# Kernel tuning notes

Hardware: AMD Instinct MI355X
Metric: run time of the kernel (lower is better)

Reference implementation:

```python
import jax, jax.numpy as jnp
import numpy as np

B, N, C_IN, C_H, C_OUT, R, X_DIM = 32, 256, 64, 128, 128, 5, 1024
NEG = -9e15

def _leaky(x, s=0.2):
    return jnp.where(x >= 0, x, s * x)

def gat_layer(atoms, mask, W, b, a):
    # atoms: (B,n,c_in), mask: (B,n,n,R) bool, W: (c_in, R*c), b: (R*c,), a: (R, 2c)
    bs, n, _ = atoms.shape
    c = a.shape[1] // 2
    h = (atoms @ W + b).reshape(bs, n, R, c)            # (B,n,R,c)
    src = jnp.einsum('bnrc,rc->bnr', h, a[:, :c])       # a . h_i part
    dst = jnp.einsum('bnrc,rc->bnr', h, a[:, c:])       # a . h_j part
    logits = _leaky(src[:, :, None, :] + dst[:, None, :, :])  # (B,i,j,R)
    masked = jnp.where(mask, logits, NEG)
    probs = jax.nn.softmax(masked.reshape(bs, n, n * R), axis=2).reshape(bs, n, n, R)
    return jnp.einsum('bijr,bjrc->bic', probs, h)       # (B,n,c)

def setup_inputs() -> dict:
    key = jax.random.key(0)
    ks = jax.random.split(key, 16)
    def p(k, shape, fan):
        return jax.random.normal(k, shape, jnp.float32) * (1.414 / np.sqrt(fan))
    inp = {
        'x': jax.random.normal(ks[0], (B, X_DIM), jnp.float32),
        'y_atoms': jax.random.normal(ks[1], (B, N, C_IN), jnp.float32),
        'y_bonds': jax.random.randint(ks[2], (B, N, N, R), 0, 2, jnp.int32),
        'W1': p(ks[3], (C_IN, R * C_H), C_IN), 'b1': jnp.zeros((R * C_H,), jnp.float32),
        'a1': p(ks[4], (R, 2 * C_H), 2 * C_H),
        'W2': p(ks[5], (C_H, R * C_H), C_H), 'b2': jnp.zeros((R * C_H,), jnp.float32),
        'a2': p(ks[6], (R, 2 * C_H), 2 * C_H),
        'W3': p(ks[7], (C_H, R * C_OUT), C_H), 'b3': jnp.zeros((R * C_OUT,), jnp.float32),
        'a3': p(ks[8], (R, 2 * C_OUT), 2 * C_OUT),
        'We1': p(ks[9], (2 * C_OUT + X_DIM, 256), 2 * C_OUT + X_DIM), 'be1': jnp.zeros((256,), jnp.float32),
        'We2': p(ks[10], (256, 32), 256), 'be2': jnp.zeros((32,), jnp.float32),
        'We3': p(ks[11], (32, 1), 32), 'be3': jnp.zeros((1,), jnp.float32),
    }
    return inp

def reference(x, y_atoms, y_bonds, W1, b1, a1, W2, b2, a2, W3, b3, a3,
              We1, be1, We2, be2, We3, be3):
    mask = (y_bonds == 1)
    h = gat_layer(y_atoms, mask, W1, b1, a1)
    h = _leaky(h)                                   # dropout is identity at eval
    h = gat_layer(h, mask, W2, b2, a2)
    h = _leaky(h)
    h = gat_layer(h, mask, W3, b3, a3)
    y_feats = jnp.concatenate([jnp.mean(h, axis=1), jnp.max(h, axis=1)], axis=1)
    z = jnp.concatenate([x, y_feats], axis=1)
    z = _leaky(z @ We1 + be1)
    z = _leaky(z @ We2 + be2)
    return z @ We3 + be3
```

## Files before the change

kernel.cpp:

```cpp
#include <hip/hip_runtime.h>
#include <cstddef>

typedef __attribute__((ext_vector_type(8))) short bf16x8;
typedef __attribute__((ext_vector_type(4))) float f32x4;

__device__ __forceinline__ float lrelu(float x) { return x >= 0.f ? x : 0.2f * x; }
__device__ __forceinline__ unsigned short f2bf(float x) {
    unsigned u = __float_as_uint(x);
    u += 0x7FFFu + ((u >> 16) & 1u);
    return (unsigned short)(u >> 16);
}

__global__ __launch_bounds__(256) void k_prepw(const float* __restrict__ W1,
                                               unsigned short* __restrict__ WT1) {
    const int nt = blockIdx.x, t = threadIdx.x;
    const int n = nt * 64 + (t & 63);
    for (int kg = t >> 6; kg < 8; kg += 4) {
        bf16x8 v;
#pragma unroll
        for (int e = 0; e < 8; ++e) v[e] = (short)f2bf(W1[(size_t)(kg * 8 + e) * 640 + n]);
        *(bf16x8*)&WT1[(size_t)n * 64 + kg * 8] = v;
    }
}

template <int K, int MODE, int EXTRA>
__global__ __launch_bounds__(256) void k_gemm_h(const float* __restrict__ Af32,
                                                const unsigned short* __restrict__ Ab,
                                                const unsigned short* __restrict__ WTg,
                                                const float* __restrict__ bias,
                                                const float* __restrict__ avec,
                                                float* __restrict__ srcp,
                                                float* __restrict__ dstp,
                                                unsigned short* __restrict__ hTf,
                                                const int* __restrict__ bonds,
                                                unsigned char* __restrict__ maskp,
                                                const float* __restrict__ W2,
                                                const float* __restrict__ W3,
                                                unsigned short* __restrict__ WT2,
                                                unsigned short* __restrict__ WT3) {
    const int t = threadIdx.x;
    const int l = blockIdx.x;
    if (EXTRA && l >= 1280) {
        int e = l - 1280;
        if (e < 2048) {
            int gt = e * 256 + t;
            const int4* p = (const int4*)(bonds + (size_t)gt * 20);
            int4 q0 = p[0], q1 = p[1], q2 = p[2], q3 = p[3], q4 = p[4];
            int v[20] = {q0.x, q0.y, q0.z, q0.w, q1.x, q1.y, q1.z, q1.w,
                         q2.x, q2.y, q2.z, q2.w, q3.x, q3.y, q3.z, q3.w,
                         q4.x, q4.y, q4.z, q4.w};
            unsigned m = 0;
#pragma unroll
            for (int k = 0; k < 4; ++k)
#pragma unroll
                for (int r = 0; r < 5; ++r)
                    m |= (v[k * 5 + r] == 1) ? (1u << (k * 8 + r)) : 0u;
            *(unsigned*)&maskp[(size_t)gt * 4] = m;
        } else {
            int e2 = e - 2048;
            const float* W = (e2 < 10) ? W2 : W3;
            unsigned short* WT = (e2 < 10) ? WT2 : WT3;
            int nt = (e2 < 10) ? e2 : e2 - 10;
            int n = nt * 64 + (t & 63);
            for (int kg = t >> 6; kg < 16; kg += 4) {
                bf16x8 v;
#pragma unroll
                for (int ee = 0; ee < 8; ++ee)
                    v[ee] = (short)f2bf(W[(size_t)(kg * 8 + ee) * 640 + n]);
                *(bf16x8*)&WT[(size_t)n * 128 + kg * 8] = v;
            }
        }
        return;
    }
    const int mt = (l & 7) * 16 + ((l >> 3) & 15);
    const int nt = l >> 7;
    const int n0 = nt * 64, m0 = mt * 64;
    const int w = t >> 6, lane = t & 63;
    const int colg = lane & 15, rquad = lane >> 4;
    const int m = m0 + w * 16 + colg;
    const int koff = rquad * 8;

    f32x4 acc[4] = {};
#pragma unroll
    for (int kk = 0; kk < K; kk += 32) {
        bf16x8 af;
        size_t off = (size_t)m * K + kk + koff;
        if (MODE == 1) {
            af = *(const bf16x8*)&Ab[off];
        } else {
            float4 q0 = *(const float4*)&Af32[off];
            float4 q1 = *(const float4*)&Af32[off + 4];
            af[0] = (short)f2bf(q0.x); af[1] = (short)f2bf(q0.y);
            af[2] = (short)f2bf(q0.z); af[3] = (short)f2bf(q0.w);
            af[4] = (short)f2bf(q1.x); af[5] = (short)f2bf(q1.y);
            af[6] = (short)f2bf(q1.z); af[7] = (short)f2bf(q1.w);
        }
#pragma unroll
        for (int ct = 0; ct < 4; ++ct) {
            bf16x8 bfv = *(const bf16x8*)&WTg[(size_t)(n0 + ct * 16 + colg) * K + kk + koff];
            acc[ct] = __builtin_amdgcn_mfma_f32_16x16x32_bf16(af, bfv, acc[ct], 0, 0, 0);
        }
    }

    const int r = n0 >> 7, chalf = n0 & 127;
    const int b = m0 >> 8, jb = m0 & 255;
    float val[4][4];
    float ssum[4] = {0.f, 0.f, 0.f, 0.f}, dsum[4] = {0.f, 0.f, 0.f, 0.f};
#pragma unroll
    for (int ct = 0; ct < 4; ++ct) {
        int cg = chalf + ct * 16 + colg;
        float bv = bias[n0 + ct * 16 + colg];
        float asr = avec[r * 256 + cg];
        float ads = avec[r * 256 + 128 + cg];
#pragma unroll
        for (int reg = 0; reg < 4; ++reg) {
            float v = acc[ct][reg] + bv;
            val[ct][reg] = v;
            ssum[reg] += v * asr;
            dsum[reg] += v * ads;
        }
    }
#pragma unroll
    for (int mk = 1; mk < 16; mk <<= 1)
#pragma unroll
        for (int reg = 0; reg < 4; ++reg) {
            ssum[reg] += __shfl_xor(ssum[reg], mk);
            dsum[reg] += __shfl_xor(dsum[reg], mk);
        }
    if (colg == 0) {
        int nhalf = (n0 >> 6) & 1;
#pragma unroll
        for (int reg = 0; reg < 4; ++reg) {
            int row = m0 + w * 16 + rquad * 4 + reg;
            srcp[nhalf * 40960 + row * 5 + r] = ssum[reg];
            dstp[nhalf * 40960 + row * 5 + r] = dsum[reg];
        }
    }
    {
        const int joct = (jb >> 3) + w * 2 + (rquad >> 1);
        const size_t tile = (size_t)((b * 5 + r) * 32 + joct) * 1024;
        const int sub = (rquad & 1) * 4;
#pragma unroll
        for (int ct = 0; ct < 4; ++ct) {
            int c = chalf + ct * 16 + colg;
            uint2 pk;
            pk.x = (unsigned)f2bf(val[ct][0]) | ((unsigned)f2bf(val[ct][1]) << 16);
            pk.y = (unsigned)f2bf(val[ct][2]) | ((unsigned)f2bf(val[ct][3]) << 16);
            *(uint2*)&hTf[tile + (size_t)c * 8 + sub] = pk;
        }
    }
}

template <int FINAL>
__global__ __launch_bounds__(512, 4) void k_agg(const unsigned short* __restrict__ hTf,
                                                const float* __restrict__ srcp,
                                                const float* __restrict__ dstp,
                                                const unsigned char* __restrict__ maskp,
                                                unsigned short* __restrict__ Ab,
                                                float* __restrict__ poolS,
                                                float* __restrict__ poolM) {
    __shared__ __align__(16) unsigned short Ps[20480];
    __shared__ __align__(16) float Ds2l[1280];
    __shared__ float Ss[80], Zw[128], Zrow[16];
    const int t = threadIdx.x;
    const int l = blockIdx.x;
    const int b = (l & 7) * 4 + ((l >> 3) & 3);
    const int itile = l >> 5;
    const int ib = b * 256 + itile * 16;
    const int w = t >> 6, lane = t & 63;
    const int colg = lane & 15, rquad = lane >> 4;
    const int c = w * 16 + colg;
    const size_t bbase = (size_t)(b * 5) * 32 * 1024;

    if (t < 80) Ss[t] = srcp[(size_t)ib * 5 + t] + srcp[40960 + (size_t)ib * 5 + t];
    for (int idx = t; idx < 1280; idx += 512) {
        int jl = idx & 255, rr = idx >> 8;
        size_t o = (size_t)(b * 256 + jl) * 5 + rr;
        Ds2l[rr * 256 + jl] = dstp[o] + dstp[40960 + o];
    }
    bf16x8 pre[4];
#pragma unroll
    for (int s = 0; s < 4; ++s)
        pre[s] = *(const bf16x8*)&hTf[bbase + (size_t)(s * 4 + rquad) * 1024 + (size_t)c * 8];
    __syncthreads();

    {
        const int i = t & 15;
        const int kq = (t >> 4) & 3;
        float esum = 0.f;
#pragma unroll
        for (int it = 0; it < 5; ++it) {
            int p = it * 512 + t;
            int s = p >> 6;
            int k0 = s * 32 + kq * 8;
            int rr = k0 >> 8, j0 = k0 & 255;
            uint2 mk8 = *(const uint2*)&maskp[((size_t)(ib + i) << 8) + j0];
            float sv = Ss[i * 5 + rr];
            float4 d0 = *(const float4*)&Ds2l[rr * 256 + j0];
            float4 d1 = *(const float4*)&Ds2l[rr * 256 + j0 + 4];
            float dv[8] = {d0.x, d0.y, d0.z, d0.w, d1.x, d1.y, d1.z, d1.w};
            bf16x8 pv;
#pragma unroll
            for (int e = 0; e < 8; ++e) {
                unsigned mb = ((e < 4 ? (mk8.x >> (8 * e)) : (mk8.y >> (8 * (e - 4)))) >> rr) & 1u;
                float vv = lrelu(sv + dv[e]);
                float ev = mb ? __expf(vv) : 0.f;
                unsigned short q = f2bf(ev);
                pv[e] = (short)q;
                esum += __uint_as_float((unsigned)q << 16);
            }
            *(bf16x8*)&Ps[p * 8] = pv;
        }
        esum += __shfl_xor(esum, 16);
        esum += __shfl_xor(esum, 32);
        if (lane < 16) Zw[w * 16 + (lane & 15)] = esum;
    }
    __syncthreads();
    if (t < 16) {
        float z = 0.f;
#pragma unroll
        for (int ww = 0; ww < 8; ++ww) z += Zw[ww * 16 + t];
        Zrow[t] = 1.f / z;
    }

    f32x4 acc0 = {}, acc1 = {};
#pragma unroll
    for (int s = 0; s < 8; ++s) {
        bf16x8 af = *(const bf16x8*)&Ps[(s * 64 + lane) * 8];
        bf16x8 bfv;
        if (s < 4) bfv = pre[s];
        else bfv = *(const bf16x8*)&hTf[bbase + (size_t)((s & 7) * 4 + rquad) * 1024 + (size_t)c * 8];
        if (s & 1) acc1 = __builtin_amdgcn_mfma_f32_16x16x32_bf16(af, bfv, acc1, 0, 0, 0);
        else       acc0 = __builtin_amdgcn_mfma_f32_16x16x32_bf16(af, bfv, acc0, 0, 0, 0);
    }
#pragma unroll 8
    for (int s = 8; s < 40; ++s) {
        bf16x8 af = *(const bf16x8*)&Ps[(s * 64 + lane) * 8];
        bf16x8 bfv = *(const bf16x8*)&hTf[bbase +
            (size_t)((s >> 3) * 32 + (s & 7) * 4 + rquad) * 1024 + (size_t)c * 8];
        if (s & 1) acc1 = __builtin_amdgcn_mfma_f32_16x16x32_bf16(af, bfv, acc1, 0, 0, 0);
        else       acc0 = __builtin_amdgcn_mfma_f32_16x16x32_bf16(af, bfv, acc0, 0, 0, 0);
    }
    __syncthreads();
    const int irow = ib + rquad * 4;
    if (FINAL) {
        float ps = 0.f, pm = -3.4e38f;
#pragma unroll
        for (int reg = 0; reg < 4; ++reg) {
            float v = (acc0[reg] + acc1[reg]) * Zrow[rquad * 4 + reg];
            ps += v;
            pm = fmaxf(pm, v);
        }
        ps += __shfl_xor(ps, 16);
        ps += __shfl_xor(ps, 32);
        pm = fmaxf(pm, __shfl_xor(pm, 16));
        pm = fmaxf(pm, __shfl_xor(pm, 32));
        if (rquad == 0) {
            poolS[(size_t)(b * 16 + itile) * 128 + c] = ps;
            poolM[(size_t)(b * 16 + itile) * 128 + c] = pm;
        }
    } else {
#pragma unroll
        for (int reg = 0; reg < 4; ++reg) {
            float v = (acc0[reg] + acc1[reg]) * Zrow[rquad * 4 + reg];
            Ab[(size_t)(irow + reg) * 128 + c] = f2bf(lrelu(v));
        }
    }
}

__global__ __launch_bounds__(256) void k_mlp1(const float* __restrict__ x,
                                              const float* __restrict__ poolS,
                                              const float* __restrict__ poolM,
                                              const float* __restrict__ We1,
                                              float* __restrict__ z1p) {
    const int kg = blockIdx.x, b = blockIdx.y;
    const int t = threadIdx.x;
    __shared__ float zs[256];
    if (kg < 4) {
        zs[t] = x[(size_t)b * 1024 + kg * 256 + t];
    } else if (t < 128) {
        float s = 0.f;
#pragma unroll
        for (int it = 0; it < 16; ++it) s += poolS[(size_t)(b * 16 + it) * 128 + t];
        zs[t] = s * (1.f / 256.f);
    } else {
        int f = t - 128;
        float mx = -3.4e38f;
#pragma unroll
        for (int it = 0; it < 16; ++it) mx = fmaxf(mx, poolM[(size_t)(b * 16 + it) * 128 + f]);
        zs[t] = mx;
    }
    __syncthreads();
    float s = 0.f;
#pragma unroll 8
    for (int k = 0; k < 256; ++k) s += zs[k] * We1[(size_t)(kg * 256 + k) * 256 + t];
    z1p[(size_t)(b * 5 + kg) * 256 + t] = s;
}

__global__ __launch_bounds__(256) void k_mlp2(const float* __restrict__ z1p,
                                              const float* __restrict__ be1,
                                              const float* __restrict__ We2,
                                              const float* __restrict__ be2,
                                              const float* __restrict__ We3,
                                              const float* __restrict__ be3,
                                              float* __restrict__ out) {
    const int b = blockIdx.x, t = threadIdx.x;
    __shared__ float z1s[256];
    __shared__ float s2p[8][32];
    __shared__ float z2s[32];
    {
        float s = be1[t];
#pragma unroll
        for (int kg = 0; kg < 5; ++kg) s += z1p[(size_t)(b * 5 + kg) * 256 + t];
        z1s[t] = lrelu(s);
    }
    __syncthreads();
    {
        int o = t & 31, g = t >> 5;
        float p = 0.f;
#pragma unroll
        for (int k = 0; k < 32; ++k) p += z1s[g * 32 + k] * We2[(g * 32 + k) * 32 + o];
        s2p[g][o] = p;
    }
    __syncthreads();
    if (t < 32) {
        float s2 = be2[t];
#pragma unroll
        for (int g = 0; g < 8; ++g) s2 += s2p[g][t];
        z2s[t] = lrelu(s2);
    }
    __syncthreads();
    if (t == 0) {
        float s3 = be3[0];
#pragma unroll
        for (int k = 0; k < 32; ++k) s3 += z2s[k] * We3[k];
        out[b] = s3;
    }
}

constexpr size_t O_MASK  = 0;
constexpr size_t O_SRCP  = 2097152;
constexpr size_t O_DSTP  = O_SRCP + 2ull * 40960 * 4;
constexpr size_t O_AB    = O_DSTP + 2ull * 40960 * 4;
constexpr size_t O_HT    = O_AB + 2097152;
constexpr size_t O_WT1   = O_HT + 5242880ull * 2;
constexpr size_t O_WT2   = O_WT1 + 640ull * 64 * 2;
constexpr size_t O_WT3   = O_WT2 + 640ull * 128 * 2;
constexpr size_t O_POOLS = O_WT3 + 640ull * 128 * 2;
constexpr size_t O_POOLM = O_POOLS + 32ull * 16 * 128 * 4;
constexpr size_t O_Z1P   = O_POOLM + 32ull * 16 * 128 * 4;

extern "C" void kernel_launch(void* const* d_in, const int* in_sizes, int n_in,
                              void* d_out, int out_size, void* d_ws, size_t ws_size,
                              hipStream_t stream) {
    const float* x       = (const float*)d_in[0];
    const float* y_atoms = (const float*)d_in[1];
    const int*   y_bonds = (const int*)d_in[2];
    const float* W1 = (const float*)d_in[3];
    const float* b1 = (const float*)d_in[4];
    const float* a1 = (const float*)d_in[5];
    const float* W2 = (const float*)d_in[6];
    const float* b2 = (const float*)d_in[7];
    const float* a2 = (const float*)d_in[8];
    const float* W3 = (const float*)d_in[9];
    const float* b3 = (const float*)d_in[10];
    const float* a3 = (const float*)d_in[11];
    const float* We1 = (const float*)d_in[12];
    const float* be1 = (const float*)d_in[13];
    const float* We2 = (const float*)d_in[14];
    const float* be2 = (const float*)d_in[15];
    const float* We3 = (const float*)d_in[16];
    const float* be3 = (const float*)d_in[17];
    float* out = (float*)d_out;

    char* ws = (char*)d_ws;
    unsigned char* maskp = (unsigned char*)(ws + O_MASK);
    float* srcp = (float*)(ws + O_SRCP);
    float* dstp = (float*)(ws + O_DSTP);
    unsigned short* Ab = (unsigned short*)(ws + O_AB);
    unsigned short* hTf = (unsigned short*)(ws + O_HT);
    unsigned short* WT1 = (unsigned short*)(ws + O_WT1);
    unsigned short* WT2 = (unsigned short*)(ws + O_WT2);
    unsigned short* WT3 = (unsigned short*)(ws + O_WT3);
    float* poolS = (float*)(ws + O_POOLS);
    float* poolM = (float*)(ws + O_POOLM);
    float* z1p   = (float*)(ws + O_Z1P);

    dim3 blk(256);

    k_prepw<<<10, blk, 0, stream>>>(W1, WT1);

    k_gemm_h<64, 0, 1><<<3348, blk, 0, stream>>>(
        y_atoms, nullptr, WT1, b1, a1, srcp, dstp, hTf,
        y_bonds, maskp, W2, W3, WT2, WT3);
    k_agg<0><<<512, dim3(512), 0, stream>>>(hTf, srcp, dstp, maskp, Ab, nullptr, nullptr);

    k_gemm_h<128, 1, 0><<<1280, blk, 0, stream>>>(
        nullptr, Ab, WT2, b2, a2, srcp, dstp, hTf,
        nullptr, nullptr, nullptr, nullptr, nullptr, nullptr);
    k_agg<0><<<512, dim3(512), 0, stream>>>(hTf, srcp, dstp, maskp, Ab, nullptr, nullptr);

    k_gemm_h<128, 1, 0><<<1280, blk, 0, stream>>>(
        nullptr, Ab, WT3, b3, a3, srcp, dstp, hTf,
        nullptr, nullptr, nullptr, nullptr, nullptr, nullptr);
    k_agg<1><<<512, dim3(512), 0, stream>>>(hTf, srcp, dstp, maskp, nullptr, poolS, poolM);

    k_mlp1<<<dim3(5, 32), blk, 0, stream>>>(x, poolS, poolM, We1, z1p);
    k_mlp2<<<32, blk, 0, stream>>>(z1p, be1, We2, be2, We3, be3, out);
}
```

Baseline: 201.9 us.

## Split aggregation K-loop across 16 waves with LDS reduction of partial accumulators

Doubles the k_agg block to 1024 threads. The two halves of the block each handle half of the 40 MFMA K-steps and combine their partial accumulators through LDS that reuses the probability buffer. The probability-generation loop is redistributed across the larger block, and the register prefetch of the first B fragments is dropped. The aim is more waves in flight per CU to hide the global hTf loads. The cost is an extra LDS round trip and barrier, with half the threads idle in the epilogue.

```diff
diff --git a/kernel.cpp b/kernel.cpp
--- a/kernel.cpp
+++ b/kernel.cpp
@@ -152,16 +152,21 @@
 }
 
 template <int FINAL>
-__global__ __launch_bounds__(512, 4) void k_agg(const unsigned short* __restrict__ hTf,
-                                                const float* __restrict__ srcp,
-                                                const float* __restrict__ dstp,
-                                                const unsigned char* __restrict__ maskp,
-                                                unsigned short* __restrict__ Ab,
-                                                float* __restrict__ poolS,
-                                                float* __restrict__ poolM) {
-    __shared__ __align__(16) unsigned short Ps[20480];
-    __shared__ __align__(16) float Ds2l[1280];
-    __shared__ float Ss[80], Zw[128], Zrow[16];
+__global__ __launch_bounds__(1024, 8) void k_agg(const unsigned short* __restrict__ hTf,
+                                                 const float* __restrict__ srcp,
+                                                 const float* __restrict__ dstp,
+                                                 const unsigned char* __restrict__ maskp,
+                                                 unsigned short* __restrict__ Ab,
+                                                 float* __restrict__ poolS,
+                                                 float* __restrict__ poolM) {
+    __shared__ __align__(16) unsigned char SM[47488];
+    unsigned short* Ps = (unsigned short*)SM;
+    float* accb = (float*)SM;
+    float* Ds2l = (float*)(SM + 40960);
+    float* Ss   = (float*)(SM + 46080);
+    float* Zw   = (float*)(SM + 46400);
+    float* Zrow = (float*)(SM + 47424);
+
     const int t = threadIdx.x;
     const int l = blockIdx.x;
     const int b = (l & 7) * 4 + ((l >> 3) & 3);
@@ -169,19 +174,14 @@
     const int ib = b * 256 + itile * 16;
     const int w = t >> 6, lane = t & 63;
     const int colg = lane & 15, rquad = lane >> 4;
-    const int c = w * 16 + colg;
     const size_t bbase = (size_t)(b * 5) * 32 * 1024;
 
     if (t < 80) Ss[t] = srcp[(size_t)ib * 5 + t] + srcp[40960 + (size_t)ib * 5 + t];
-    for (int idx = t; idx < 1280; idx += 512) {
+    for (int idx = t; idx < 1280; idx += 1024) {
         int jl = idx & 255, rr = idx >> 8;
         size_t o = (size_t)(b * 256 + jl) * 5 + rr;
         Ds2l[rr * 256 + jl] = dstp[o] + dstp[40960 + o];
     }
-    bf16x8 pre[4];
-#pragma unroll
-    for (int s = 0; s < 4; ++s)
-        pre[s] = *(const bf16x8*)&hTf[bbase + (size_t)(s * 4 + rquad) * 1024 + (size_t)c * 8];
     __syncthreads();
 
     {
@@ -189,27 +189,29 @@
         const int kq = (t >> 4) & 3;
         float esum = 0.f;
 #pragma unroll
-        for (int it = 0; it < 5; ++it) {
-            int p = it * 512 + t;
-            int s = p >> 6;
-            int k0 = s * 32 + kq * 8;
-            int rr = k0 >> 8, j0 = k0 & 255;
-            uint2 mk8 = *(const uint2*)&maskp[((size_t)(ib + i) << 8) + j0];
-            float sv = Ss[i * 5 + rr];
-            float4 d0 = *(const float4*)&Ds2l[rr * 256 + j0];
-            float4 d1 = *(const float4*)&Ds2l[rr * 256 + j0 + 4];
-            float dv[8] = {d0.x, d0.y, d0.z, d0.w, d1.x, d1.y, d1.z, d1.w};
-            bf16x8 pv;
-#pragma unroll
-            for (int e = 0; e < 8; ++e) {
-                unsigned mb = ((e < 4 ? (mk8.x >> (8 * e)) : (mk8.y >> (8 * (e - 4)))) >> rr) & 1u;
-                float vv = lrelu(sv + dv[e]);
-                float ev = mb ? __expf(vv) : 0.f;
-                unsigned short q = f2bf(ev);
-                pv[e] = (short)q;
-                esum += __uint_as_float((unsigned)q << 16);
+        for (int it = 0; it < 3; ++it) {
+            int p = it * 1024 + t;
+            if (p < 2560) {
+                int s = p >> 6;
+                int k0 = s * 32 + kq * 8;
+                int rr = k0 >> 8, j0 = k0 & 255;
+                uint2 mk8 = *(const uint2*)&maskp[((size_t)(ib + i) << 8) + j0];
+                float sv = Ss[i * 5 + rr];
+                float4 d0 = *(const float4*)&Ds2l[rr * 256 + j0];
+                float4 d1 = *(const float4*)&Ds2l[rr * 256 + j0 + 4];
+                float dv[8] = {d0.x, d0.y, d0.z, d0.w, d1.x, d1.y, d1.z, d1.w};
+                bf16x8 pv;
+#pragma unroll
+                for (int e = 0; e < 8; ++e) {
+                    unsigned mb = ((e < 4 ? (mk8.x >> (8 * e)) : (mk8.y >> (8 * (e - 4)))) >> rr) & 1u;
+                    float vv = lrelu(sv + dv[e]);
+                    float ev = mb ? __expf(vv) : 0.f;
+                    unsigned short q = f2bf(ev);
+                    pv[e] = (short)q;
+                    esum += __uint_as_float((unsigned)q << 16);
+                }
+                *(bf16x8*)&Ps[p * 8] = pv;
             }
-            *(bf16x8*)&Ps[p * 8] = pv;
         }
         esum += __shfl_xor(esum, 16);
         esum += __shfl_xor(esum, 32);
@@ -219,51 +221,56 @@
     if (t < 16) {
         float z = 0.f;
 #pragma unroll
-        for (int ww = 0; ww < 8; ++ww) z += Zw[ww * 16 + t];
+        for (int ww = 0; ww < 16; ++ww) z += Zw[ww * 16 + t];
         Zrow[t] = 1.f / z;
     }
 
+    const int c = (w & 7) * 16 + colg;
+    const int sbase = (w >> 3) * 20;
     f32x4 acc0 = {}, acc1 = {};
-#pragma unroll
-    for (int s = 0; s < 8; ++s) {
-        bf16x8 af = *(const bf16x8*)&Ps[(s * 64 + lane) * 8];
-        bf16x8 bfv;
-        if (s < 4) bfv = pre[s];
-        else bfv = *(const bf16x8*)&hTf[bbase + (size_t)((s & 7) * 4 + rquad) * 1024 + (size_t)c * 8];
-        if (s & 1) acc1 = __builtin_amdgcn_mfma_f32_16x16x32_bf16(af, bfv, acc1, 0, 0, 0);
-        else       acc0 = __builtin_amdgcn_mfma_f32_16x16x32_bf16(af, bfv, acc0, 0, 0, 0);
-    }
-#pragma unroll 8
-    for (int s = 8; s < 40; ++s) {
+#pragma unroll 4
+    for (int q = 0; q < 20; ++q) {
+        int s = sbase + q;
         bf16x8 af = *(const bf16x8*)&Ps[(s * 64 + lane) * 8];
         bf16x8 bfv = *(const bf16x8*)&hTf[bbase +
             (size_t)((s >> 3) * 32 + (s & 7) * 4 + rquad) * 1024 + (size_t)c * 8];
-        if (s & 1) acc1 = __builtin_amdgcn_mfma_f32_16x16x32_bf16(af, bfv, acc1, 0, 0, 0);
+        if (q & 1) acc1 = __builtin_amdgcn_mfma_f32_16x16x32_bf16(af, bfv, acc1, 0, 0, 0);
         else       acc0 = __builtin_amdgcn_mfma_f32_16x16x32_bf16(af, bfv, acc0, 0, 0, 0);
     }
     __syncthreads();
-    const int irow = ib + rquad * 4;
-    if (FINAL) {
-        float ps = 0.f, pm = -3.4e38f;
-#pragma unroll
-        for (int reg = 0; reg < 4; ++reg) {
-            float v = (acc0[reg] + acc1[reg]) * Zrow[rquad * 4 + reg];
-            ps += v;
-            pm = fmaxf(pm, v);
-        }
-        ps += __shfl_xor(ps, 16);
-        ps += __shfl_xor(ps, 32);
-        pm = fmaxf(pm, __shfl_xor(pm, 16));
-        pm = fmaxf(pm, __shfl_xor(pm, 32));
-        if (rquad == 0) {
-            poolS[(size_t)(b * 16 + itile) * 128 + c] = ps;
-            poolM[(size_t)(b * 16 + itile) * 128 + c] = pm;
-        }
-    } else {
-#pragma unroll
-        for (int reg = 0; reg < 4; ++reg) {
-            float v = (acc0[reg] + acc1[reg]) * Zrow[rquad * 4 + reg];
-            Ab[(size_t)(irow + reg) * 128 + c] = f2bf(lrelu(v));
+    {
+        f32x4 ac;
+#pragma unroll
+        for (int reg = 0; reg < 4; ++reg) ac[reg] = acc0[reg] + acc1[reg];
+        *(f32x4*)&accb[(size_t)(w * 64 + lane) * 4] = ac;
+    }
+    __syncthreads();
+    if (t < 512) {
+        f32x4 pa = *(const f32x4*)&accb[(size_t)(w * 64 + lane) * 4];
+        f32x4 pb = *(const f32x4*)&accb[(size_t)((w + 8) * 64 + lane) * 4];
+        const int irow = ib + rquad * 4;
+        if (FINAL) {
+            float ps = 0.f, pm = -3.4e38f;
+#pragma unroll
+            for (int reg = 0; reg < 4; ++reg) {
+                float v = (pa[reg] + pb[reg]) * Zrow[rquad * 4 + reg];
+                ps += v;
+                pm = fmaxf(pm, v);
+            }
+            ps += __shfl_xor(ps, 16);
+            ps += __shfl_xor(ps, 32);
+            pm = fmaxf(pm, __shfl_xor(pm, 16));
+            pm = fmaxf(pm, __shfl_xor(pm, 32));
+            if (rquad == 0) {
+                poolS[(size_t)(b * 16 + itile) * 128 + c] = ps;
+                poolM[(size_t)(b * 16 + itile) * 128 + c] = pm;
+            }
+        } else {
+#pragma unroll
+            for (int reg = 0; reg < 4; ++reg) {
+                float v = (pa[reg] + pb[reg]) * Zrow[rquad * 4 + reg];
+                Ab[(size_t)(irow + reg) * 128 + c] = f2bf(lrelu(v));
+            }
         }
     }
 }
@@ -393,17 +400,17 @@
     k_gemm_h<64, 0, 1><<<3348, blk, 0, stream>>>(
         y_atoms, nullptr, WT1, b1, a1, srcp, dstp, hTf,
         y_bonds, maskp, W2, W3, WT2, WT3);
-    k_agg<0><<<512, dim3(512), 0, stream>>>(hTf, srcp, dstp, maskp, Ab, nullptr, nullptr);
+    k_agg<0><<<512, dim3(1024), 0, stream>>>(hTf, srcp, dstp, maskp, Ab, nullptr, nullptr);
 
     k_gemm_h<128, 1, 0><<<1280, blk, 0, stream>>>(
         nullptr, Ab, WT2, b2, a2, srcp, dstp, hTf,
         nullptr, nullptr, nullptr, nullptr, nullptr, nullptr);
-    k_agg<0><<<512, dim3(512), 0, stream>>>(hTf, srcp, dstp, maskp, Ab, nullptr, nullptr);
+    k_agg<0><<<512, dim3(1024), 0, stream>>>(hTf, srcp, dstp, maskp, Ab, nullptr, nullptr);
 
     k_gemm_h<128, 1, 0><<<1280, blk, 0, stream>>>(
         nullptr, Ab, WT3, b3, a3, srcp, dstp, hTf,
         nullptr, nullptr, nullptr, nullptr, nullptr, nullptr);
-    k_agg<1><<<512, dim3(512), 0, stream>>>(hTf, srcp, dstp, maskp, nullptr, poolS, poolM);
+    k_agg<1><<<512, dim3(1024), 0, stream>>>(hTf, srcp, dstp, maskp, nullptr, poolS, poolM);
 
     k_mlp1<<<dim3(5, 32), blk, 0, stream>>>(x, poolS, poolM, We1, z1p);
     k_mlp2<<<32, blk, 0, stream>>>(z1p, be1, We2, be2, We3, be3, out);
```

New measurement: 206.5 us. 2.3% more time.
